# Performance work log

Measured on AMD Instinct MI355X. Metric: run time of the kernel, lower is better.

Reference implementation:

```python
import jax, jax.numpy as jnp
import numpy as np

H = 16        # num_attention_heads
D = 1024      # hidden_size
HD = D // H   # head_dim = 64


def setup_inputs() -> dict:
    key = jax.random.key(0)
    ks = jax.random.split(key, 5)
    B, T = 16, 1024
    s_in = 1.0 / np.sqrt(D)
    return {
        "hidden_states": jax.random.normal(ks[0], (B, T, D), dtype=jnp.float32),
        "w_qkv": jax.random.normal(ks[1], (D, 3 * D), dtype=jnp.float32) * s_in,
        "b_qkv": jnp.zeros((3 * D,), dtype=jnp.float32),
        "w_out": jax.random.normal(ks[2], (D, D), dtype=jnp.float32) * s_in,
        "b_out": jnp.zeros((D,), dtype=jnp.float32),
    }


def reference(hidden_states, w_qkv, b_qkv, w_out, b_out):
    B, T, C = hidden_states.shape
    qkv = hidden_states @ w_qkv + b_qkv                      # [B,T,3C]
    q, k, v = jnp.split(qkv, 3, axis=-1)
    # [B,T,C] -> [B,H,T,HD]
    q = q.reshape(B, T, H, HD).transpose(0, 2, 1, 3)
    k = k.reshape(B, T, H, HD).transpose(0, 2, 1, 3)
    v = v.reshape(B, T, H, HD).transpose(0, 2, 1, 3)
    scale = 1.0 / np.sqrt(HD)
    logits = jnp.einsum("bhqd,bhkd->bhqk", q, k) * scale     # [B,H,T,T]
    attn = jax.nn.softmax(logits, axis=-1)
    out = jnp.einsum("bhqk,bhkd->bhqd", attn, v)             # [B,H,T,HD]
    out = out.transpose(0, 2, 1, 3).reshape(B, T, C)
    return out @ w_out + b_out
```

## Files before the change

kernel.cpp:

```cpp
#include <hip/hip_runtime.h>
#include <cstdint>
#include <cstddef>

typedef _Float16 h8 __attribute__((ext_vector_type(8)));
typedef _Float16 h4 __attribute__((ext_vector_type(4)));
typedef float f4 __attribute__((ext_vector_type(4)));

#define MFMA(a, b, c) __builtin_amdgcn_mfma_f32_16x16x32_f16((a), (b), (c), 0, 0, 0)

__device__ __forceinline__ void gl_lds16(const void* g, void* l) {
  __builtin_amdgcn_global_load_lds((const __attribute__((address_space(1))) void*)g,
                                   (__attribute__((address_space(3))) void*)l, 16, 0, 0);
}

__device__ __forceinline__ h8 lds_frag(const char* base, int r, int ch) {
  return *(const h8*)(base + ((r * 8 + (ch ^ (r & 7))) * 16));
}

__device__ __forceinline__ void BAR() {
  asm volatile("" ::: "memory");
  __builtin_amdgcn_s_barrier();
  asm volatile("" ::: "memory");
}

__global__ void k_cvt_hs(const float* __restrict__ in, _Float16* __restrict__ out, int n8) {
  int i = blockIdx.x * blockDim.x + threadIdx.x;
  if (i >= n8) return;
  size_t idx = (size_t)i * 8;
  float4 a = *(const float4*)(in + idx);
  float4 b = *(const float4*)(in + idx + 4);
  h8 o;
  o[0] = (_Float16)a.x; o[1] = (_Float16)a.y; o[2] = (_Float16)a.z; o[3] = (_Float16)a.w;
  o[4] = (_Float16)b.x; o[5] = (_Float16)b.y; o[6] = (_Float16)b.z; o[7] = (_Float16)b.w;
  *(h8*)(out + idx) = o;
}

__global__ void k_transcvt(const float* __restrict__ in, _Float16* __restrict__ out, int N, int K) {
  __shared__ float tile[64 * 65];
  int tn = blockIdx.x * 64, tk = blockIdx.y * 64;
  for (int i = 0; i < 4; ++i) {
    int cid = i * 256 + threadIdx.x;
    int r = cid >> 4, c4 = cid & 15;
    float4 v = *(const float4*)(in + (size_t)(tk + r) * N + tn + c4 * 4);
    tile[r * 65 + c4 * 4 + 0] = v.x; tile[r * 65 + c4 * 4 + 1] = v.y;
    tile[r * 65 + c4 * 4 + 2] = v.z; tile[r * 65 + c4 * 4 + 3] = v.w;
  }
  __syncthreads();
  for (int i = 0; i < 2; ++i) {
    int cid = i * 256 + threadIdx.x;
    int n = cid >> 3, kc = cid & 7;
    h8 o;
    for (int j = 0; j < 8; ++j) o[j] = (_Float16)tile[(kc * 8 + j) * 65 + n];
    *(h8*)(out + (size_t)(tn + n) * K + tk + kc * 8) = o;
  }
}

__device__ __forceinline__ void gemm256_mainloop(
    const _Float16* __restrict__ A, const _Float16* __restrict__ BT,
    char* smem, int tm, int tn, f4 (&acc)[8][4]) {
  int tid = threadIdx.x, lane = tid & 63, wave = tid >> 6;
  int l15 = lane & 15, l4 = lane >> 4;
  int wm = (wave >> 2) * 128, wn = (wave & 3) * 64;
  const _Float16* Ab = A + (size_t)tm * 1024;
  const _Float16* Bb = BT + (size_t)tn * 1024;
  int r0 = tid >> 3, cg = (tid & 7) ^ (r0 & 7);
  char* cA = smem;           char* nA = smem + 32768;
  char* cB = smem + 65536;   char* nB = smem + 98304;

  auto stA = [&](int kt, int h, char* dst) {
    const _Float16* s = Ab + (size_t)(h * 128 + r0) * 1024 + kt + cg * 8;
    gl_lds16(s, dst + h * 16384 + tid * 16);
    gl_lds16(s + 64 * 1024, dst + h * 16384 + 8192 + tid * 16);
  };
  auto stB = [&](int kt, int h, char* dst) {
    const _Float16* s = Bb + (size_t)(h * 128 + r0) * 1024 + kt + cg * 8;
    gl_lds16(s, dst + h * 16384 + tid * 16);
    gl_lds16(s + 64 * 1024, dst + h * 16384 + 8192 + tid * 16);
  };

  stA(0, 0, cA); stA(0, 1, cA);
  stB(0, 0, cB); stB(0, 1, cB);
  stB(64, 0, nB); stB(64, 1, nB);
  asm volatile("s_waitcnt vmcnt(4)" ::: "memory");
  BAR();

  h8 af[4][2], bf[4][2];
  for (int u = 0; u < 16; ++u) {
    int kt1 = (u + 1) << 6, kt2 = (u + 2) << 6;
#pragma unroll
    for (int mi = 0; mi < 4; ++mi) {
      int r = wm + mi * 16 + l15;
      af[mi][0] = lds_frag(cA, r, l4);
      af[mi][1] = lds_frag(cA, r, 4 + l4);
    }
#pragma unroll
    for (int nj = 0; nj < 2; ++nj) {
      int r = wn + nj * 16 + l15;
      bf[nj][0] = lds_frag(cB, r, l4);
      bf[nj][1] = lds_frag(cB, r, 4 + l4);
    }
    if (u < 15) stA(kt1, 0, nA);
    asm volatile("s_waitcnt lgkmcnt(8)" ::: "memory");
    BAR();
    asm volatile("s_waitcnt lgkmcnt(0)" ::: "memory");
    __builtin_amdgcn_s_setprio(1);
#pragma unroll
    for (int kk = 0; kk < 2; ++kk)
#pragma unroll
      for (int mi = 0; mi < 4; ++mi)
#pragma unroll
        for (int nj = 0; nj < 2; ++nj)
          acc[mi][nj] = MFMA(af[mi][kk], bf[nj][kk], acc[mi][nj]);
    __builtin_amdgcn_s_setprio(0);
    BAR();
#pragma unroll
    for (int nj = 2; nj < 4; ++nj) {
      int r = wn + nj * 16 + l15;
      bf[nj][0] = lds_frag(cB, r, l4);
      bf[nj][1] = lds_frag(cB, r, 4 + l4);
    }
    if (u < 15) stA(kt1, 1, nA);
    BAR();
    asm volatile("s_waitcnt lgkmcnt(0)" ::: "memory");
    __builtin_amdgcn_s_setprio(1);
#pragma unroll
    for (int kk = 0; kk < 2; ++kk)
#pragma unroll
      for (int mi = 0; mi < 4; ++mi)
#pragma unroll
        for (int nj = 2; nj < 4; ++nj)
          acc[mi][nj] = MFMA(af[mi][kk], bf[nj][kk], acc[mi][nj]);
    __builtin_amdgcn_s_setprio(0);
    BAR();
#pragma unroll
    for (int mi = 0; mi < 4; ++mi) {
      int r = wm + 64 + mi * 16 + l15;
      af[mi][0] = lds_frag(cA, r, l4);
      af[mi][1] = lds_frag(cA, r, 4 + l4);
    }
    if (u < 14) stB(kt2, 0, cB);
    BAR();
    asm volatile("s_waitcnt lgkmcnt(0)" ::: "memory");
    __builtin_amdgcn_s_setprio(1);
#pragma unroll
    for (int kk = 0; kk < 2; ++kk)
#pragma unroll
      for (int mi = 0; mi < 4; ++mi)
#pragma unroll
        for (int nj = 2; nj < 4; ++nj)
          acc[4 + mi][nj] = MFMA(af[mi][kk], bf[nj][kk], acc[4 + mi][nj]);
    __builtin_amdgcn_s_setprio(0);
    BAR();
    if (u < 14) stB(kt2, 1, cB);
    if (u < 14) asm volatile("s_waitcnt vmcnt(4)" ::: "memory");
    else        asm volatile("s_waitcnt vmcnt(0)" ::: "memory");
    BAR();
    __builtin_amdgcn_s_setprio(1);
#pragma unroll
    for (int kk = 0; kk < 2; ++kk)
#pragma unroll
      for (int mi = 0; mi < 4; ++mi)
#pragma unroll
        for (int nj = 0; nj < 2; ++nj)
          acc[4 + mi][nj] = MFMA(af[mi][kk], bf[nj][kk], acc[4 + mi][nj]);
    __builtin_amdgcn_s_setprio(0);
    BAR();
    char* t = cA; cA = nA; nA = t;
    t = cB; cB = nB; nB = t;
  }
}

__global__ __launch_bounds__(512) void k_gemm_qkv(
    const _Float16* __restrict__ A, const _Float16* __restrict__ BT,
    const float* __restrict__ bias,
    _Float16* __restrict__ Q, _Float16* __restrict__ Kq, _Float16* __restrict__ Vt) {
  __shared__ char smem[131072];
  int id = blockIdx.x;
  int swz = (id & 7) * 96 + (id >> 3);
  int by = swz / 12, bx = swz - by * 12;
  int tm = by * 256, tn = bx * 256;
  f4 acc[8][4] = {};
  gemm256_mainloop(A, BT, smem, tm, tn, acc);

  int tid = threadIdx.x, lane = tid & 63, wave = tid >> 6;
  int l15 = lane & 15, l4 = lane >> 4;
  int wm = (wave >> 2) * 128, wn = (wave & 3) * 64;
  if (tn < 2048) {
    _Float16* dst = (tn >= 1024) ? Kq : Q;
#pragma unroll
    for (int nj = 0; nj < 4; ++nj) {
      int n = tn + wn + nj * 16 + l15;
      float bv = bias[n];
      int h = (n >> 6) & 15, d = n & 63;
#pragma unroll
      for (int mig = 0; mig < 8; ++mig) {
#pragma unroll
        for (int r = 0; r < 4; ++r) {
          int m = tm + wm + mig * 16 + l4 * 4 + r;
          int b = m >> 10, t = m & 1023;
          dst[(((size_t)b * 16 + h) * 1024 + t) * 64 + d] =
              (_Float16)(acc[mig][nj][r] + bv);
        }
      }
    }
  } else {
    _Float16* L = (_Float16*)smem;
    int b = tm >> 10, tb = tm & 1023;
#pragma unroll
    for (int p = 0; p < 2; ++p) {
      __syncthreads();
      if (((wave >> 1) & 1) == p) {
        int nloc = (wave & 1) * 64;
#pragma unroll
        for (int nj = 0; nj < 4; ++nj) {
          int nl = nloc + nj * 16 + l15;
          float bv = bias[tn + p * 128 + nl];
#pragma unroll
          for (int mig = 0; mig < 8; ++mig) {
            h4 pk;
#pragma unroll
            for (int r = 0; r < 4; ++r) pk[r] = (_Float16)(acc[mig][nj][r] + bv);
            *(h4*)(L + nl * 264 + wm + mig * 16 + l4 * 4) = pk;
          }
        }
      }
      __syncthreads();
#pragma unroll
      for (int i = 0; i < 8; ++i) {
        int cid = i * 512 + tid;
        int nl = cid >> 5, tc = cid & 31;
        int ng = tn + p * 128 + nl;
        int h = (ng >> 6) & 15, d = ng & 63;
        *(h8*)(Vt + (((size_t)b * 16 + h) * 64 + d) * 1024 + tb + tc * 8) =
            *(const h8*)(L + nl * 264 + tc * 8);
      }
    }
  }
}

__global__ __launch_bounds__(256, 2) void k_attn(
    const _Float16* __restrict__ Q, const _Float16* __restrict__ Kk,
    const _Float16* __restrict__ Vt, _Float16* __restrict__ O) {
  __shared__ char smem[32768 + 8192 + 8192];
  _Float16* sQ = (_Float16*)smem;
  _Float16* sP = (_Float16*)smem;
  _Float16* sK = (_Float16*)(smem + 32768);
  _Float16* sV = (_Float16*)(smem + 32768 + 8192);
  const float SCL = 0.125f * 1.44269504088896340736f;
  int tid = threadIdx.x, wave = tid >> 6, lane = tid & 63;
  int l15 = lane & 15, l4 = lane >> 4;
  int bh = blockIdx.y;
  int qt = blockIdx.x * 256;
  const _Float16* Qb = Q + (size_t)bh * 65536;
  const _Float16* Kb = Kk + (size_t)bh * 65536;
  const _Float16* Vb = Vt + (size_t)bh * 65536;

  for (int i = 0; i < 8; ++i) {
    int cid = i * 256 + tid;
    int r = cid >> 3, cs = cid & 7, cg = cs ^ (r & 7);
    gl_lds16(Qb + (size_t)(qt + r) * 64 + cg * 8, (char*)sQ + cid * 16);
  }
  __syncthreads();
  h8 qf[4][2];
  for (int nt = 0; nt < 4; ++nt) {
    int r = wave * 64 + nt * 16 + l15;
    for (int kk = 0; kk < 2; ++kk) {
      int ch = kk * 4 + l4;
      qf[nt][kk] = *(const h8*)((const char*)sQ + ((r * 8 + (ch ^ (r & 7))) * 16));
    }
  }
  _Float16 scl_h = (_Float16)SCL;
  for (int nt = 0; nt < 4; ++nt)
    for (int kk = 0; kk < 2; ++kk)
      for (int j = 0; j < 8; ++j) qf[nt][kk][j] *= scl_h;

  int cid0 = tid, cid1 = tid + 256;
  int r0 = cid0 >> 3, c0 = (cid0 & 7) ^ (r0 & 7);
  int r1 = cid1 >> 3, c1 = (cid1 & 7) ^ (r1 & 7);
  const _Float16* kp0 = Kb + (size_t)r0 * 64 + c0 * 8;
  const _Float16* kp1 = Kb + (size_t)r1 * 64 + c1 * 8;
  const _Float16* vp0 = Vb + (size_t)r0 * 1024 + c0 * 8;
  const _Float16* vp1 = Vb + (size_t)r1 * 1024 + c1 * 8;
  char* dK0 = (char*)sK + cid0 * 16; char* dK1 = (char*)sK + cid1 * 16;
  char* dV0 = (char*)sV + cid0 * 16; char* dV1 = (char*)sV + cid1 * 16;

  f4 oacc[4][4] = {};
  f4 lacc[4] = {};
  h8 ones;
  for (int j = 0; j < 8; ++j) ones[j] = (_Float16)1.0f;
  _Float16* pw = sP + wave * 64 * 40;

  for (int kt = 0; kt < 1024; kt += 64) {
    __syncthreads();
    gl_lds16(kp0, dK0); gl_lds16(kp1, dK1);
    gl_lds16(vp0, dV0); gl_lds16(vp1, dV1);
    kp0 += 4096; kp1 += 4096; vp0 += 64; vp1 += 64;
    __syncthreads();
    for (int mh = 0; mh < 2; ++mh) {
      f4 sacc[2][4] = {};
      for (int kk = 0; kk < 2; ++kk) {
        h8 kf[2];
        int ch = kk * 4 + l4;
        for (int mt = 0; mt < 2; ++mt) {
          int r = mh * 32 + mt * 16 + l15;
          kf[mt] = *(const h8*)((const char*)sK + ((r * 8 + (ch ^ (r & 7))) * 16));
        }
        for (int mt = 0; mt < 2; ++mt)
          for (int nt = 0; nt < 4; ++nt)
            sacc[mt][nt] = MFMA(kf[mt], qf[nt][kk], sacc[mt][nt]);
      }
      for (int mt = 0; mt < 2; ++mt) {
        for (int nt = 0; nt < 4; ++nt) {
          float p0 = exp2f(sacc[mt][nt][0]);
          float p1 = exp2f(sacc[mt][nt][1]);
          float p2 = exp2f(sacc[mt][nt][2]);
          float p3 = exp2f(sacc[mt][nt][3]);
          h4 pk;
          pk[0] = (_Float16)p0; pk[1] = (_Float16)p1;
          pk[2] = (_Float16)p2; pk[3] = (_Float16)p3;
          *(h4*)(pw + (nt * 16 + l15) * 40 + mt * 16 + l4 * 4) = pk;
        }
      }
      h8 pf[4], vf[4];
      for (int mi = 0; mi < 4; ++mi)
        pf[mi] = *(const h8*)(pw + (mi * 16 + l15) * 40 + l4 * 8);
      int ch = mh * 4 + l4;
      for (int nd = 0; nd < 4; ++nd) {
        int r = nd * 16 + l15;
        vf[nd] = *(const h8*)((const char*)sV + ((r * 8 + (ch ^ (r & 7))) * 16));
      }
      for (int mi = 0; mi < 4; ++mi) {
        for (int nd = 0; nd < 4; ++nd)
          oacc[mi][nd] = MFMA(pf[mi], vf[nd], oacc[mi][nd]);
        lacc[mi] = MFMA(pf[mi], ones, lacc[mi]);
      }
    }
  }
  int b = bh >> 4, h = bh & 15;
  for (int mi = 0; mi < 4; ++mi) {
    for (int r = 0; r < 4; ++r) {
      float inv = 1.f / lacc[mi][r];
      int t = qt + wave * 64 + mi * 16 + l4 * 4 + r;
      for (int nd = 0; nd < 4; ++nd)
        O[(size_t)(b * 1024 + t) * 1024 + h * 64 + nd * 16 + l15] =
            (_Float16)(oacc[mi][nd][r] * inv);
    }
  }
}

__global__ __launch_bounds__(512) void k_gemm_out(
    const _Float16* __restrict__ A, const _Float16* __restrict__ BT,
    const float* __restrict__ bias, float* __restrict__ C) {
  __shared__ char smem[131072];
  int id = blockIdx.x;
  int swz = (id & 7) * 32 + (id >> 3);
  int by = swz >> 2, bx = swz & 3;
  int tm = by * 256, tn = bx * 256;
  f4 acc[8][4] = {};
  gemm256_mainloop(A, BT, smem, tm, tn, acc);

  int tid = threadIdx.x, lane = tid & 63, wave = tid >> 6;
  int l15 = lane & 15, l4 = lane >> 4;
  int wm = (wave >> 2) * 128, wn = (wave & 3) * 64;
#pragma unroll
  for (int nj = 0; nj < 4; ++nj) {
    int n = tn + wn + nj * 16 + l15;
    float bv = bias[n];
#pragma unroll
    for (int mig = 0; mig < 8; ++mig) {
#pragma unroll
      for (int r = 0; r < 4; ++r) {
        int m = tm + wm + mig * 16 + l4 * 4 + r;
        C[(size_t)m * 1024 + n] = acc[mig][nj][r] + bv;
      }
    }
  }
}

extern "C" void kernel_launch(void* const* d_in, const int* in_sizes, int n_in,
                              void* d_out, int out_size, void* d_ws, size_t ws_size,
                              hipStream_t stream) {
  const float* hs    = (const float*)d_in[0];
  const float* w_qkv = (const float*)d_in[1];
  const float* b_qkv = (const float*)d_in[2];
  const float* w_out = (const float*)d_in[3];
  const float* b_out = (const float*)d_in[4];
  float* out = (float*)d_out;
  char* ws = (char*)d_ws;

  _Float16* hs_h  = (_Float16*)(ws);
  _Float16* wqkvT = (_Float16*)(ws + 33554432);
  _Float16* woutT = (_Float16*)(ws + 39845888);
  _Float16* q_ws  = (_Float16*)(ws + 41943040);
  _Float16* k_ws  = (_Float16*)(ws + 75497472);
  _Float16* vt_ws = (_Float16*)(ws + 109051904);

  k_cvt_hs<<<8192, 256, 0, stream>>>(hs, hs_h, 2097152);
  k_transcvt<<<dim3(48, 16), 256, 0, stream>>>(w_qkv, wqkvT, 3072, 1024);
  k_transcvt<<<dim3(16, 16), 256, 0, stream>>>(w_out, woutT, 1024, 1024);
  k_gemm_qkv<<<768, 512, 0, stream>>>(hs_h, wqkvT, b_qkv, q_ws, k_ws, vt_ws);
  _Float16* attn_h = hs_h;
  k_attn<<<dim3(4, 256), 256, 0, stream>>>(q_ws, k_ws, vt_ws, attn_h);
  k_gemm_out<<<256, 512, 0, stream>>>(attn_h, woutT, b_out, out);
}
```

Before: 388.3 us.

## Double-buffer K/V tiles in attention and load Q directly to registers

```diff
diff --git a/kernel.cpp b/kernel.cpp
--- a/kernel.cpp
+++ b/kernel.cpp
@@ -238,14 +238,12 @@
   }
 }
 
-__global__ __launch_bounds__(256, 2) void k_attn(
+__global__ __launch_bounds__(256, 3) void k_attn(
     const _Float16* __restrict__ Q, const _Float16* __restrict__ Kk,
     const _Float16* __restrict__ Vt, _Float16* __restrict__ O) {
-  __shared__ char smem[32768 + 8192 + 8192];
-  _Float16* sQ = (_Float16*)smem;
+  __shared__ char smem[20480 + 32768];
   _Float16* sP = (_Float16*)smem;
-  _Float16* sK = (_Float16*)(smem + 32768);
-  _Float16* sV = (_Float16*)(smem + 32768 + 8192);
+  char* sKV = smem + 20480;
   const float SCL = 0.125f * 1.44269504088896340736f;
   int tid = threadIdx.x, wave = tid >> 6, lane = tid & 63;
   int l15 = lane & 15, l4 = lane >> 4;
@@ -255,23 +253,20 @@
   const _Float16* Kb = Kk + (size_t)bh * 65536;
   const _Float16* Vb = Vt + (size_t)bh * 65536;
 
-  for (int i = 0; i < 8; ++i) {
-    int cid = i * 256 + tid;
-    int r = cid >> 3, cs = cid & 7, cg = cs ^ (r & 7);
-    gl_lds16(Qb + (size_t)(qt + r) * 64 + cg * 8, (char*)sQ + cid * 16);
-  }
-  __syncthreads();
   h8 qf[4][2];
+#pragma unroll
   for (int nt = 0; nt < 4; ++nt) {
-    int r = wave * 64 + nt * 16 + l15;
-    for (int kk = 0; kk < 2; ++kk) {
-      int ch = kk * 4 + l4;
-      qf[nt][kk] = *(const h8*)((const char*)sQ + ((r * 8 + (ch ^ (r & 7))) * 16));
-    }
+    int r = qt + wave * 64 + nt * 16 + l15;
+#pragma unroll
+    for (int kk = 0; kk < 2; ++kk)
+      qf[nt][kk] = *(const h8*)(Qb + (size_t)r * 64 + (kk * 4 + l4) * 8);
   }
   _Float16 scl_h = (_Float16)SCL;
+#pragma unroll
   for (int nt = 0; nt < 4; ++nt)
-    for (int kk = 0; kk < 2; ++kk)
+#pragma unroll
+    for (int kk = 0; kk < 2; ++kk)
+#pragma unroll
       for (int j = 0; j < 8; ++j) qf[nt][kk][j] *= scl_h;
 
   int cid0 = tid, cid1 = tid + 256;
@@ -281,35 +276,54 @@
   const _Float16* kp1 = Kb + (size_t)r1 * 64 + c1 * 8;
   const _Float16* vp0 = Vb + (size_t)r0 * 1024 + c0 * 8;
   const _Float16* vp1 = Vb + (size_t)r1 * 1024 + c1 * 8;
-  char* dK0 = (char*)sK + cid0 * 16; char* dK1 = (char*)sK + cid1 * 16;
-  char* dV0 = (char*)sV + cid0 * 16; char* dV1 = (char*)sV + cid1 * 16;
+
+  auto stage = [&](int it, int b) {
+    char* dK = sKV + b * 16384;
+    char* dV = dK + 8192;
+    size_t ko = (size_t)it * 4096;
+    size_t vo = (size_t)it * 64;
+    gl_lds16(kp0 + ko, dK + cid0 * 16);
+    gl_lds16(kp1 + ko, dK + cid1 * 16);
+    gl_lds16(vp0 + vo, dV + cid0 * 16);
+    gl_lds16(vp1 + vo, dV + cid1 * 16);
+  };
 
   f4 oacc[4][4] = {};
   f4 lacc[4] = {};
   h8 ones;
+#pragma unroll
   for (int j = 0; j < 8; ++j) ones[j] = (_Float16)1.0f;
   _Float16* pw = sP + wave * 64 * 40;
 
-  for (int kt = 0; kt < 1024; kt += 64) {
-    __syncthreads();
-    gl_lds16(kp0, dK0); gl_lds16(kp1, dK1);
-    gl_lds16(vp0, dV0); gl_lds16(vp1, dV1);
-    kp0 += 4096; kp1 += 4096; vp0 += 64; vp1 += 64;
-    __syncthreads();
+  stage(0, 0);
+  asm volatile("s_waitcnt vmcnt(0)" ::: "memory");
+  BAR();
+
+  for (int it = 0; it < 16; ++it) {
+    int cur = it & 1;
+    if (it < 15) stage(it + 1, cur ^ 1);
+    const char* sK = sKV + cur * 16384;
+    const char* sV = sK + 8192;
     for (int mh = 0; mh < 2; ++mh) {
       f4 sacc[2][4] = {};
+#pragma unroll
       for (int kk = 0; kk < 2; ++kk) {
         h8 kf[2];
         int ch = kk * 4 + l4;
+#pragma unroll
         for (int mt = 0; mt < 2; ++mt) {
           int r = mh * 32 + mt * 16 + l15;
-          kf[mt] = *(const h8*)((const char*)sK + ((r * 8 + (ch ^ (r & 7))) * 16));
+          kf[mt] = *(const h8*)(sK + ((r * 8 + (ch ^ (r & 7))) * 16));
         }
+#pragma unroll
         for (int mt = 0; mt < 2; ++mt)
+#pragma unroll
           for (int nt = 0; nt < 4; ++nt)
             sacc[mt][nt] = MFMA(kf[mt], qf[nt][kk], sacc[mt][nt]);
       }
+#pragma unroll
       for (int mt = 0; mt < 2; ++mt) {
+#pragma unroll
         for (int nt = 0; nt < 4; ++nt) {
           float p0 = exp2f(sacc[mt][nt][0]);
           float p1 = exp2f(sacc[mt][nt][1]);
@@ -322,25 +336,34 @@
         }
       }
       h8 pf[4], vf[4];
+#pragma unroll
       for (int mi = 0; mi < 4; ++mi)
         pf[mi] = *(const h8*)(pw + (mi * 16 + l15) * 40 + l4 * 8);
       int ch = mh * 4 + l4;
+#pragma unroll
       for (int nd = 0; nd < 4; ++nd) {
         int r = nd * 16 + l15;
-        vf[nd] = *(const h8*)((const char*)sV + ((r * 8 + (ch ^ (r & 7))) * 16));
-      }
+        vf[nd] = *(const h8*)(sV + ((r * 8 + (ch ^ (r & 7))) * 16));
+      }
+#pragma unroll
       for (int mi = 0; mi < 4; ++mi) {
+#pragma unroll
         for (int nd = 0; nd < 4; ++nd)
           oacc[mi][nd] = MFMA(pf[mi], vf[nd], oacc[mi][nd]);
         lacc[mi] = MFMA(pf[mi], ones, lacc[mi]);
       }
     }
+    asm volatile("s_waitcnt vmcnt(0) lgkmcnt(0)" ::: "memory");
+    BAR();
   }
   int b = bh >> 4, h = bh & 15;
+#pragma unroll
   for (int mi = 0; mi < 4; ++mi) {
+#pragma unroll
     for (int r = 0; r < 4; ++r) {
       float inv = 1.f / lacc[mi][r];
       int t = qt + wave * 64 + mi * 16 + l4 * 4 + r;
+#pragma unroll
       for (int nd = 0; nd < 4; ++nd)
         O[(size_t)(b * 1024 + t) * 1024 + h * 64 + nd * 16 + l15] =
             (_Float16)(oacc[mi][nd][r] * inv);
```

Result: slower. 444.3 us (+14.4%).
